# Kernel tuning notes

Measured on AMD Instinct MI355X. Metric: run time of the kernel, lower is better.

Reference implementation:

```python
import jax, jax.numpy as jnp
import numpy as np

PI = np.pi


def setup_inputs() -> dict:
    key = jax.random.key(0)
    ks = jax.random.split(key, 20)
    B, L, D = 2, 1024, 512
    TP = 16      # n_sets(4) * planes_per_set(4)
    PP = 16      # pos_planes
    MAXL = 8192
    sc = 1.0 / np.sqrt(D)
    return {
        "x": jax.random.normal(ks[0], (B, L, D), jnp.float32),
        "Wk": jax.random.normal(ks[1], (TP, D), jnp.float32) * sc,
        "bk": jnp.zeros((TP,), jnp.float32),
        "Wq": jax.random.normal(ks[2], (TP, D), jnp.float32) * sc,
        "bq": jnp.zeros((TP,), jnp.float32),
        "Wv": jax.random.normal(ks[3], (D, D), jnp.float32) * sc,
        "bv": jnp.zeros((D,), jnp.float32),
        "ln_g": jnp.ones((D,), jnp.float32),
        "ln_b": jnp.zeros((D,), jnp.float32),
        "Wo": jax.random.normal(ks[4], (D, D), jnp.float32) * sc,
        "bo": jnp.zeros((D,), jnp.float32),
        "set_w": jnp.ones((4,), jnp.float32),
        "pos_phases": jax.random.normal(ks[5], (MAXL, PP), jnp.float32) * PI,
        "pos_weight": jnp.ones((1,), jnp.float32),
        "Wg1": jax.random.normal(ks[6], (D // 2, D), jnp.float32) * sc,
        "bg1": jnp.zeros((D // 2,), jnp.float32),
        "Wg2": jax.random.normal(ks[7], (1, D // 2), jnp.float32) * np.sqrt(2.0 / D),
        "bg2": jnp.zeros((1,), jnp.float32),
    }


def reference(x, Wk, bk, Wq, bq, Wv, bv, ln_g, ln_b, Wo, bo,
              set_w, pos_phases, pos_weight, Wg1, bg1, Wg2, bg2):
    B, L, D = x.shape
    n_sets, pps = 4, 4

    # --- content phasor memory ---
    kp = jnp.tanh(x @ Wk.T + bk) * PI                       # [B,L,16]
    qp = jnp.tanh(x @ Wq.T + bq) * PI
    key_ph = jnp.exp(1j * kp).reshape(B, L, n_sets, pps)    # [B,L,S,P] c64
    qry_ph = jnp.exp(1j * qp).reshape(B, L, n_sets, pps)
    Vr = x @ Wv.T + bv                                       # [B,L,D]
    V = Vr.astype(jnp.complex64)

    bound = key_ph[..., None] * V[:, :, None, None, :]       # [B,L,S,P,D] c64
    mem = jnp.cumsum(bound, axis=1)                          # prefix-sum memory
    retr = (mem * jnp.conj(qry_ph)[..., None]).sum(axis=3).real   # [B,L,S,D]
    w = jax.nn.softmax(set_w)
    content = (retr * w[None, None, :, None]).sum(axis=2)    # [B,L,D]

    # --- positional cos/sin memory ---
    ph = pos_phases[:L]                                      # [L,PP]
    c = jnp.cos(ph)[None]                                    # [1,L,PP]
    s = jnp.sin(ph)[None]
    br = Vr[:, :, None, :] * c[..., None]                    # [B,L,PP,D]
    bi = Vr[:, :, None, :] * s[..., None]
    mr = jnp.cumsum(br, axis=1)
    mi = jnp.cumsum(bi, axis=1)
    pos = (mr * c[..., None] + mi * s[..., None]).sum(axis=2)  # [B,L,D]

    # --- gate, mix, normalize, output proj ---
    g = jax.nn.sigmoid(
        jax.nn.gelu(x @ Wg1.T + bg1, approximate=False) @ Wg2.T + bg2)  # [B,L,1]
    total = g * content + (1.0 - g) * jax.nn.sigmoid(pos_weight) * pos
    norm = jnp.sqrt(jnp.arange(1, L + 1, dtype=x.dtype) * pps)[None, :, None]
    t = total / norm
    mu = t.mean(-1, keepdims=True)
    var = ((t - mu) ** 2).mean(-1, keepdims=True)
    tn = (t - mu) / jnp.sqrt(var + 1e-5) * ln_g + ln_b
    return x + tn @ Wo.T + bo
```

## Files before the change

kernel.cpp:

```cpp
#include <hip/hip_runtime.h>
#include <math.h>

#define PI_F 3.14159265358979323846f
#define BB 2
#define LL 1024
#define NCH 64
#define CHUNK 32
#define NCHUNK (LL/CHUNK)
#define NW 1408
#define YH 384

typedef __attribute__((ext_vector_type(8))) short short8;
typedef __attribute__((ext_vector_type(4))) float floatx4;
typedef const __attribute__((address_space(1))) unsigned int cgu32;
typedef __attribute__((address_space(3))) unsigned int lu32;

__device__ __forceinline__ unsigned short f2bf(float f){
    unsigned u = __float_as_uint(f);
    unsigned r = (u + 0x7fff + ((u >> 16) & 1)) >> 16;
    return (unsigned short)r;
}

__global__ __launch_bounds__(128) void k_prep(
    const float* __restrict__ Wv, const float* __restrict__ Wg1,
    const float* __restrict__ Wk, const float* __restrict__ Wq,
    const float* __restrict__ Wo,
    const float* __restrict__ bv, const float* __restrict__ bg1,
    const float* __restrict__ bk, const float* __restrict__ bq,
    const float* __restrict__ bo, const float* __restrict__ x,
    unsigned short* __restrict__ Wb, float* __restrict__ bcat,
    unsigned short* __restrict__ xb)
{
    const int bid = blockIdx.x, tid = threadIdx.x;
    if (bid < NW){
        const int n = bid;
        const float* src = (n<512) ? Wv  + (size_t)n*512
                         : (n<768) ? Wg1 + (size_t)(n-512)*512
                         : (n<784) ? Wk  + (size_t)(n-768)*512
                         : (n<800) ? Wq  + (size_t)(n-784)*512
                         : (n<896) ? (const float*)0
                                   : Wo  + (size_t)(n-896)*512;
        float4 v = make_float4(0.f,0.f,0.f,0.f);
        if (src) v = ((const float4*)src)[tid];
        ushort4 o; o.x=f2bf(v.x); o.y=f2bf(v.y); o.z=f2bf(v.z); o.w=f2bf(v.w);
        ((ushort4*)(Wb + (size_t)n*512))[tid] = o;
        if (tid == 0)
            bcat[n] = (n<512)?bv[n] : (n<768)?bg1[n-512] : (n<784)?bk[n-768]
                    : (n<800)?bq[n-784] : (n<896)?0.f : bo[n-896];
    } else {
        const size_t i = (size_t)(bid - NW)*128 + tid;
        float4 v = ((const float4*)x)[i];
        ushort4 o; o.x=f2bf(v.x); o.y=f2bf(v.y); o.z=f2bf(v.z); o.w=f2bf(v.w);
        ((ushort4*)xb)[i] = o;
    }
}

__device__ __forceinline__ void gemm64x64(
    const unsigned short* Ag, const unsigned short* Bg,
    short* As, short* Bs, int tid, floatx4 acc[2][2])
{
    const int lane = tid & 63, w = tid >> 6;
    const int wm = w & 1, wn = w >> 1;
    const int q = lane >> 4, m15 = lane & 15;
    for (int kt = 0; kt < 512; kt += 64) {
        __syncthreads();
        #pragma unroll
        for (int i = 0; i < 2; ++i) {
            const int rowbase = (w*2 + i) * 8;
            const int r  = rowbase + (lane >> 3);
            const int gb = (lane & 7) ^ (r & 7);
            const unsigned short* ga  = Ag + (size_t)r*512 + kt + gb*8;
            const unsigned short* gbp = Bg + (size_t)r*512 + kt + gb*8;
            __builtin_amdgcn_global_load_lds((cgu32*)(const void*)ga,
                                             (lu32*)(As + rowbase*64), 16, 0, 0);
            __builtin_amdgcn_global_load_lds((cgu32*)(const void*)gbp,
                                             (lu32*)(Bs + rowbase*64), 16, 0, 0);
        }
        __syncthreads();
        #pragma unroll
        for (int k32 = 0; k32 < 64; k32 += 32) {
            short8 af[2], bf[2];
            #pragma unroll
            for (int t = 0; t < 2; ++t) {
                const int ra  = 32*wm + 16*t + m15;
                const int sba = ((k32>>3) + q) ^ (ra & 7);
                af[t] = *(const short8*)(As + ra*64 + sba*8);
                const int rb  = 32*wn + 16*t + m15;
                const int sbb = ((k32>>3) + q) ^ (rb & 7);
                bf[t] = *(const short8*)(Bs + rb*64 + sbb*8);
            }
            #pragma unroll
            for (int mt = 0; mt < 2; ++mt)
                #pragma unroll
                for (int nt = 0; nt < 2; ++nt)
                    acc[mt][nt] = __builtin_amdgcn_mfma_f32_16x16x32_bf16(
                        af[mt], bf[nt], acc[mt][nt], 0, 0, 0);
        }
    }
}

__global__ __launch_bounds__(256) void kg1(
    const unsigned short* __restrict__ xb, const unsigned short* __restrict__ Wb,
    const float* __restrict__ bcat, unsigned short* __restrict__ Vt,
    float* __restrict__ Yh)
{
    __shared__ short As[64*64], Bs[64*64];
    const int tid = threadIdx.x;
    const int row0 = blockIdx.x*64, n0 = blockIdx.y*64;
    floatx4 acc[2][2];
    #pragma unroll
    for (int mt=0;mt<2;++mt)
        #pragma unroll
        for (int nt=0;nt<2;++nt) acc[mt][nt] = (floatx4){0.f,0.f,0.f,0.f};
    gemm64x64(xb + (size_t)row0*512, Wb + (size_t)n0*512, As, Bs, tid, acc);
    const int lane = tid & 63, w = tid >> 6;
    const int wm = w & 1, wn = w >> 1, q = lane >> 4, m15 = lane & 15;
    if (n0 < 512){
        const int b = row0 >> 10, lb = row0 & 1023;
        #pragma unroll
        for (int mt=0;mt<2;++mt)
            #pragma unroll
            for (int nt=0;nt<2;++nt){
                const int d = n0 + 32*wn + 16*nt + m15;
                const float bb = bcat[d];
                const int l0 = lb + 32*wm + 16*mt + q*4;
                ushort4 o;
                o.x = f2bf(acc[mt][nt][0] + bb);
                o.y = f2bf(acc[mt][nt][1] + bb);
                o.z = f2bf(acc[mt][nt][2] + bb);
                o.w = f2bf(acc[mt][nt][3] + bb);
                *(ushort4*)(Vt + ((size_t)(b*512 + d))*1024 + l0) = o;
            }
    } else {
        #pragma unroll
        for (int mt=0;mt<2;++mt)
            #pragma unroll
            for (int nt=0;nt<2;++nt){
                const int n = n0 + 32*wn + 16*nt + m15;
                const float bb = bcat[n];
                #pragma unroll
                for (int reg=0;reg<4;++reg){
                    const int m = row0 + 32*wm + 16*mt + q*4 + reg;
                    Yh[(size_t)m*YH + (n-512)] = acc[mt][nt][reg] + bb;
                }
            }
    }
}

__global__ __launch_bounds__(256) void k_act(
    const float* __restrict__ Yh, const float* __restrict__ Wg2,
    const float* __restrict__ bg2, const float* __restrict__ set_w,
    const float* __restrict__ pos_phases, const float* __restrict__ pos_weight,
    unsigned short* __restrict__ ab, unsigned short* __restrict__ Rb,
    unsigned short* __restrict__ aT)
{
    const int tid = threadIdx.x, lane = tid & 63, w = tid >> 6;
    const int row0 = blockIdx.x * 8;
    float s0=set_w[0], s1=set_w[1], s2=set_w[2], s3=set_w[3];
    float m = fmaxf(fmaxf(s0,s1), fmaxf(s2,s3));
    float e0=expf(s0-m), e1=expf(s1-m), e2=expf(s2-m), e3=expf(s3-m);
    float esum = e0+e1+e2+e3;
    float spw = 1.f/(1.f+expf(-pos_weight[0]));
    float b2 = bg2[0];
    #pragma unroll
    for (int rr=0;rr<2;++rr){
        int row = row0 + w + 4*rr;
        const float* yrow = Yh + (size_t)row*YH;
        float hs = 0.f;
        #pragma unroll
        for (int i=0;i<4;++i){
            float hv = yrow[lane + 64*i];
            float ge = 0.5f*hv*(1.f + erff(hv*0.70710678118f));
            hs += ge * Wg2[lane + 64*i];
        }
        #pragma unroll
        for (int off=32; off; off>>=1) hs += __shfl_xor(hs, off, 64);
        float g = 1.f/(1.f+expf(-(hs + b2)));
        if (lane < 16){
            int j = lane;
            int l = row & (LL-1);
            int b = row >> 10;
            float kang = PI_F*tanhf(yrow[256 + j]);
            float qang = PI_F*tanhf(yrow[272 + j]);
            float wsm = (j<4?e0: j<8?e1: j<12?e2: e3) / esum;
            float rnorm = 1.f/(2.f*sqrtf((float)(l+1)));
            float av[4], rv[4];
            av[0] = cosf(kang); av[1] = sinf(kang);
            float cw = g*wsm*rnorm;
            rv[0] = cw*cosf(qang); rv[1] = cw*sinf(qang);
            float ph = pos_phases[(size_t)l*16 + j];
            float pc = cosf(ph), ps = sinf(ph);
            av[2] = pc; av[3] = ps;
            float cp = (1.f-g)*spw*rnorm;
            rv[2] = cp*pc; rv[3] = cp*ps;
            unsigned short* arow = ab + (size_t)row*NCH;
            unsigned short* Rrow = Rb + (size_t)row*NCH;
            #pragma unroll
            for (int t=0;t<4;++t){
                arow[16*t + j] = f2bf(av[t]);
                Rrow[16*t + j] = f2bf(rv[t]);
                aT[((size_t)b*NCH + 16*t + j)*1024 + l] = f2bf(av[t]);
            }
        }
    }
}

__global__ __launch_bounds__(256) void k2a_chunksum(
    const unsigned short* __restrict__ aT, const unsigned short* __restrict__ Vt,
    float* __restrict__ P)
{
    const int c = blockIdx.x, b = blockIdx.y, z = blockIdx.z;
    const int tid = threadIdx.x, lane = tid & 63, w = tid >> 6;
    const int q = lane >> 4, m15 = lane & 15;
    short8 af[4];
    #pragma unroll
    for (int mt=0;mt<4;++mt)
        af[mt] = *(const short8*)(aT + ((size_t)b*NCH + 16*mt + m15)*1024 + c*32 + q*8);
    floatx4 acc[4][4];
    #pragma unroll
    for (int mt=0;mt<4;++mt)
        #pragma unroll
        for (int nt=0;nt<4;++nt) acc[mt][nt] = (floatx4){0.f,0.f,0.f,0.f};
    #pragma unroll
    for (int nt=0;nt<4;++nt){
        const int d = z*256 + w*64 + 16*nt + m15;
        short8 bf = *(const short8*)(Vt + ((size_t)(b*512 + d))*1024 + c*32 + q*8);
        #pragma unroll
        for (int mt=0;mt<4;++mt)
            acc[mt][nt] = __builtin_amdgcn_mfma_f32_16x16x32_bf16(af[mt], bf, acc[mt][nt], 0,0,0);
    }
    float* Pc = P + ((size_t)(b*NCHUNK + c))*512*NCH;
    #pragma unroll
    for (int mt=0;mt<4;++mt)
        #pragma unroll
        for (int nt=0;nt<4;++nt){
            const int d = z*256 + w*64 + 16*nt + m15;
            const int ch0 = 16*mt + q*4;
            *(floatx4*)(Pc + (size_t)d*NCH + ch0) = acc[mt][nt];
        }
}

__global__ __launch_bounds__(256) void k2b_prefix(
    const float* __restrict__ P, unsigned short* __restrict__ S0t)
{
    const int b = blockIdx.y;
    const size_t idx = (size_t)blockIdx.x*256 + threadIdx.x;
    float run = 0.f;
    for (int c=0;c<NCHUNK;++c){
        const size_t o = ((size_t)(b*NCHUNK + c))*512*NCH + idx;
        float v = P[o];
        S0t[o] = f2bf(run);
        run += v;
    }
}

__global__ __launch_bounds__(256) void k2c_scan(
    const unsigned short* __restrict__ ab, const unsigned short* __restrict__ Rb,
    const unsigned short* __restrict__ Vt, const unsigned short* __restrict__ S0t,
    const float* __restrict__ ln_g, const float* __restrict__ ln_b,
    unsigned short* __restrict__ Tn)
{
    __shared__ short Msh[32*32];
    __shared__ float Tsh[32*512];
    const int c = blockIdx.x, b = blockIdx.y;
    const int tid = threadIdx.x, lane = tid & 63, w = tid >> 6;
    const int q = lane >> 4, m15 = lane & 15;
    const int grow = b*1024 + c*32;

    if (w == 0){
        floatx4 mcc[2][2];
        #pragma unroll
        for (int mt=0;mt<2;++mt)
            #pragma unroll
            for (int nt=0;nt<2;++nt) mcc[mt][nt] = (floatx4){0.f,0.f,0.f,0.f};
        #pragma unroll
        for (int ks=0;ks<2;++ks){
            short8 ra[2], bb[2];
            #pragma unroll
            for (int t=0;t<2;++t){
                ra[t] = *(const short8*)(Rb + (size_t)(grow + 16*t + m15)*NCH + ks*32 + q*8);
                bb[t] = *(const short8*)(ab + (size_t)(grow + 16*t + m15)*NCH + ks*32 + q*8);
            }
            #pragma unroll
            for (int mt=0;mt<2;++mt)
                #pragma unroll
                for (int nt=0;nt<2;++nt)
                    mcc[mt][nt] = __builtin_amdgcn_mfma_f32_16x16x32_bf16(
                        ra[mt], bb[nt], mcc[mt][nt], 0,0,0);
        }
        #pragma unroll
        for (int mt=0;mt<2;++mt)
            #pragma unroll
            for (int nt=0;nt<2;++nt){
                const int nl = 16*nt + m15;
                #pragma unroll
                for (int reg=0;reg<4;++reg){
                    const int ml = 16*mt + q*4 + reg;
                    Msh[ml*32 + nl] = (nl <= ml) ? (short)f2bf(mcc[mt][nt][reg]) : (short)0;
                }
            }
    }
    __syncthreads();

    short8 a1[2], a2[2][2];
    #pragma unroll
    for (int mt=0;mt<2;++mt){
        a1[mt] = *(const short8*)(Msh + (16*mt + m15)*32 + q*8);
        #pragma unroll
        for (int ks=0;ks<2;++ks)
            a2[ks][mt] = *(const short8*)(Rb + (size_t)(grow + 16*mt + m15)*NCH + ks*32 + q*8);
    }
    floatx4 acc[2][8];
    #pragma unroll
    for (int mt=0;mt<2;++mt)
        #pragma unroll
        for (int nt=0;nt<8;++nt) acc[mt][nt] = (floatx4){0.f,0.f,0.f,0.f};
    const unsigned short* S0c = S0t + ((size_t)(b*NCHUNK + c))*512*NCH;
    #pragma unroll
    for (int nt=0;nt<8;++nt){
        const int d = w*128 + 16*nt + m15;
        short8 b1 = *(const short8*)(Vt + ((size_t)(b*512 + d))*1024 + c*32 + q*8);
        #pragma unroll
        for (int mt=0;mt<2;++mt)
            acc[mt][nt] = __builtin_amdgcn_mfma_f32_16x16x32_bf16(a1[mt], b1, acc[mt][nt], 0,0,0);
        #pragma unroll
        for (int ks=0;ks<2;++ks){
            short8 b2 = *(const short8*)(S0c + (size_t)d*NCH + ks*32 + q*8);
            #pragma unroll
            for (int mt=0;mt<2;++mt)
                acc[mt][nt] = __builtin_amdgcn_mfma_f32_16x16x32_bf16(a2[ks][mt], b2, acc[mt][nt], 0,0,0);
        }
    }
    #pragma unroll
    for (int mt=0;mt<2;++mt)
        #pragma unroll
        for (int nt=0;nt<8;++nt){
            const int d = w*128 + 16*nt + m15;
            #pragma unroll
            for (int reg=0;reg<4;++reg)
                Tsh[(16*mt + q*4 + reg)*512 + d] = acc[mt][nt][reg];
        }
    __syncthreads();

    #pragma unroll
    for (int i=0;i<8;++i){
        const int r = w*8 + i;
        float s=0.f, sq=0.f;
        #pragma unroll
        for (int t=0;t<8;++t){
            float v = Tsh[r*512 + lane + 64*t];
            s += v; sq += v*v;
        }
        #pragma unroll
        for (int off=32; off; off>>=1){
            s += __shfl_xor(s, off, 64); sq += __shfl_xor(sq, off, 64);
        }
        float mu  = s*(1.f/512.f);
        float var = sq*(1.f/512.f) - mu*mu;
        float rsd = rsqrtf(var + 1e-5f);
        unsigned short* trow = Tn + (size_t)(grow + r)*512;
        #pragma unroll
        for (int t=0;t<8;++t){
            const int d = lane + 64*t;
            float v = (Tsh[r*512 + d] - mu)*rsd*ln_g[d] + ln_b[d];
            trow[d] = f2bf(v);
        }
    }
}

__global__ __launch_bounds__(256) void kg2(
    const unsigned short* __restrict__ Tn, const unsigned short* __restrict__ Wb,
    const float* __restrict__ bcat, const float* __restrict__ x,
    float* __restrict__ out)
{
    __shared__ short As[64*64], Bs[64*64];
    const int tid = threadIdx.x;
    const int row0 = blockIdx.x*64, n0 = blockIdx.y*64;
    floatx4 acc[2][2];
    #pragma unroll
    for (int mt=0;mt<2;++mt)
        #pragma unroll
        for (int nt=0;nt<2;++nt) acc[mt][nt] = (floatx4){0.f,0.f,0.f,0.f};
    gemm64x64(Tn + (size_t)row0*512, Wb + (size_t)(896+n0)*512, As, Bs, tid, acc);
    const int lane = tid & 63, w = tid >> 6;
    const int wm = w & 1, wn = w >> 1, q = lane >> 4, m15 = lane & 15;
    #pragma unroll
    for (int mt=0;mt<2;++mt)
        #pragma unroll
        for (int nt=0;nt<2;++nt){
            const int n = n0 + 32*wn + 16*nt + m15;
            const float bb = bcat[896 + n];
            #pragma unroll
            for (int reg=0;reg<4;++reg){
                const int m = row0 + 32*wm + 16*mt + q*4 + reg;
                out[(size_t)m*512 + n] = x[(size_t)m*512 + n] + acc[mt][nt][reg] + bb;
            }
        }
}

extern "C" void kernel_launch(void* const* d_in, const int* in_sizes, int n_in,
                              void* d_out, int out_size, void* d_ws, size_t ws_size,
                              hipStream_t stream) {
    const float* x    = (const float*)d_in[0];
    const float* Wk   = (const float*)d_in[1];
    const float* bk   = (const float*)d_in[2];
    const float* Wq   = (const float*)d_in[3];
    const float* bq   = (const float*)d_in[4];
    const float* Wv   = (const float*)d_in[5];
    const float* bv   = (const float*)d_in[6];
    const float* ln_g = (const float*)d_in[7];
    const float* ln_b = (const float*)d_in[8];
    const float* Wo   = (const float*)d_in[9];
    const float* bo   = (const float*)d_in[10];
    const float* set_w      = (const float*)d_in[11];
    const float* pos_phases = (const float*)d_in[12];
    const float* pos_weight = (const float*)d_in[13];
    const float* Wg1  = (const float*)d_in[14];
    const float* bg1  = (const float*)d_in[15];
    const float* Wg2  = (const float*)d_in[16];
    const float* bg2  = (const float*)d_in[17];
    float* out = (float*)d_out;

    float* ws   = (float*)d_ws;
    float* Yh   = ws;
    float* P    = Yh + (size_t)2048*YH;
    float* bcat = P  + (size_t)BB*NCHUNK*512*NCH;
    unsigned short* Wb  = (unsigned short*)(bcat + NW);
    unsigned short* xb  = Wb  + (size_t)NW*512;
    unsigned short* Vt  = xb  + (size_t)2048*512;
    unsigned short* ab  = Vt  + (size_t)BB*512*1024;
    unsigned short* Rb  = ab  + (size_t)2048*NCH;
    unsigned short* aT  = Rb  + (size_t)2048*NCH;
    unsigned short* S0t = aT  + (size_t)BB*NCH*1024;
    unsigned short* Tn  = S0t + (size_t)BB*NCHUNK*512*NCH;

    k_prep<<<dim3(NW + 2048), 128, 0, stream>>>(
        Wv,Wg1,Wk,Wq,Wo, bv,bg1,bk,bq,bo, x, Wb, bcat, xb);
    kg1<<<dim3(2048/64, 14), 256, 0, stream>>>(xb, Wb, bcat, Vt, Yh);
    k_act<<<dim3(2048/8), 256, 0, stream>>>(
        Yh, Wg2, bg2, set_w, pos_phases, pos_weight, ab, Rb, aT);
    k2a_chunksum<<<dim3(NCHUNK, BB, 2), 256, 0, stream>>>(aT, Vt, P);
    k2b_prefix<<<dim3(512*NCH/256, BB), 256, 0, stream>>>(P, S0t);
    k2c_scan<<<dim3(NCHUNK, BB), 256, 0, stream>>>(ab, Rb, Vt, S0t, ln_g, ln_b, Tn);
    kg2<<<dim3(2048/64, 512/64), 256, 0, stream>>>(Tn, Wb, bcat, x, out);
}
```

Measured before the change: 135.2 us.

## Fuse six stage kernels into one persistent kernel with grid-wide barriers

Replaces the six kernels that followed the prep kernel (GEMM1, activation, chunk sums, prefix, scan with layernorm, GEMM2) with one persistent 512-block kernel. The stages are separated by atomic-counter grid barriers, which the prep kernel resets. This removes five kernel launches and the gaps between them. In exchange, many blocks sit idle in the later stages, and the design needs all 512 blocks to be co-resident, which the 67KB of static shared memory and launch bounds of 2 may not allow on every configuration. The chunk-sum stage is also re-split so each block does a quarter of the previous work.

```diff
diff --git a/kernel.cpp b/kernel.cpp
--- a/kernel.cpp
+++ b/kernel.cpp
@@ -9,6 +9,7 @@
 #define NCHUNK (LL/CHUNK)
 #define NW 1408
 #define YH 384
+#define GRID_F 512
 
 typedef __attribute__((ext_vector_type(8))) short short8;
 typedef __attribute__((ext_vector_type(4))) float floatx4;
@@ -29,9 +30,10 @@
     const float* __restrict__ bk, const float* __restrict__ bq,
     const float* __restrict__ bo, const float* __restrict__ x,
     unsigned short* __restrict__ Wb, float* __restrict__ bcat,
-    unsigned short* __restrict__ xb)
+    unsigned short* __restrict__ xb, unsigned* __restrict__ bar)
 {
     const int bid = blockIdx.x, tid = threadIdx.x;
+    if (bid == 0 && tid < 8) bar[tid] = 0u;
     if (bid < NW){
         const int n = bid;
         const float* src = (n<512) ? Wv  + (size_t)n*512
@@ -55,12 +57,23 @@
     }
 }
 
+__device__ __forceinline__ void gsync(unsigned* bar, unsigned nblk){
+    __syncthreads();
+    if (threadIdx.x == 0){
+        __threadfence();
+        __hip_atomic_fetch_add(bar, 1u, __ATOMIC_RELAXED, __HIP_MEMORY_SCOPE_AGENT);
+        while (__hip_atomic_load(bar, __ATOMIC_RELAXED, __HIP_MEMORY_SCOPE_AGENT) < nblk)
+            __builtin_amdgcn_s_sleep(2);
+        __threadfence();
+    }
+    __syncthreads();
+}
+
 __device__ __forceinline__ void gemm64x64(
     const unsigned short* Ag, const unsigned short* Bg,
     short* As, short* Bs, int tid, floatx4 acc[2][2])
 {
     const int lane = tid & 63, w = tid >> 6;
-    const int wm = w & 1, wn = w >> 1;
     const int q = lane >> 4, m15 = lane & 15;
     for (int kt = 0; kt < 512; kt += 64) {
         __syncthreads();
@@ -82,10 +95,10 @@
             short8 af[2], bf[2];
             #pragma unroll
             for (int t = 0; t < 2; ++t) {
-                const int ra  = 32*wm + 16*t + m15;
+                const int ra  = 32*(w & 1) + 16*t + m15;
                 const int sba = ((k32>>3) + q) ^ (ra & 7);
                 af[t] = *(const short8*)(As + ra*64 + sba*8);
-                const int rb  = 32*wn + 16*t + m15;
+                const int rb  = 32*(w >> 1) + 16*t + m15;
                 const int sbb = ((k32>>3) + q) ^ (rb & 7);
                 bf[t] = *(const short8*)(Bs + rb*64 + sbb*8);
             }
@@ -99,72 +112,78 @@
     }
 }
 
-__global__ __launch_bounds__(256) void kg1(
+__global__ __launch_bounds__(256, 2) void k_fused(
     const unsigned short* __restrict__ xb, const unsigned short* __restrict__ Wb,
     const float* __restrict__ bcat, unsigned short* __restrict__ Vt,
-    float* __restrict__ Yh)
+    float* __restrict__ Yh,
+    const float* __restrict__ Wg2, const float* __restrict__ bg2,
+    const float* __restrict__ set_w, const float* __restrict__ pos_phases,
+    const float* __restrict__ pos_weight,
+    unsigned short* __restrict__ ab, unsigned short* __restrict__ Rb,
+    unsigned short* __restrict__ aT,
+    float* __restrict__ P, unsigned short* __restrict__ S0t,
+    const float* __restrict__ ln_g, const float* __restrict__ ln_b,
+    unsigned short* __restrict__ Tn,
+    const float* __restrict__ x, float* __restrict__ out,
+    unsigned* __restrict__ bar)
 {
-    __shared__ short As[64*64], Bs[64*64];
-    const int tid = threadIdx.x;
-    const int row0 = blockIdx.x*64, n0 = blockIdx.y*64;
-    floatx4 acc[2][2];
-    #pragma unroll
-    for (int mt=0;mt<2;++mt)
-        #pragma unroll
-        for (int nt=0;nt<2;++nt) acc[mt][nt] = (floatx4){0.f,0.f,0.f,0.f};
-    gemm64x64(xb + (size_t)row0*512, Wb + (size_t)n0*512, As, Bs, tid, acc);
+    __shared__ __align__(16) char smem[67584];
+    const int bid = blockIdx.x, tid = threadIdx.x;
     const int lane = tid & 63, w = tid >> 6;
-    const int wm = w & 1, wn = w >> 1, q = lane >> 4, m15 = lane & 15;
-    if (n0 < 512){
-        const int b = row0 >> 10, lb = row0 & 1023;
+    const int q = lane >> 4, m15 = lane & 15;
+
+    if (bid < 448){
+        short* As = (short*)smem;
+        short* Bs = (short*)(smem + 8192);
+        const int row0 = (bid & 31)*64, n0 = (bid >> 5)*64;
+        floatx4 acc[2][2];
         #pragma unroll
         for (int mt=0;mt<2;++mt)
             #pragma unroll
-            for (int nt=0;nt<2;++nt){
-                const int d = n0 + 32*wn + 16*nt + m15;
-                const float bb = bcat[d];
-                const int l0 = lb + 32*wm + 16*mt + q*4;
-                ushort4 o;
-                o.x = f2bf(acc[mt][nt][0] + bb);
-                o.y = f2bf(acc[mt][nt][1] + bb);
-                o.z = f2bf(acc[mt][nt][2] + bb);
-                o.w = f2bf(acc[mt][nt][3] + bb);
-                *(ushort4*)(Vt + ((size_t)(b*512 + d))*1024 + l0) = o;
-            }
-    } else {
-        #pragma unroll
-        for (int mt=0;mt<2;++mt)
-            #pragma unroll
-            for (int nt=0;nt<2;++nt){
-                const int n = n0 + 32*wn + 16*nt + m15;
-                const float bb = bcat[n];
-                #pragma unroll
-                for (int reg=0;reg<4;++reg){
-                    const int m = row0 + 32*wm + 16*mt + q*4 + reg;
-                    Yh[(size_t)m*YH + (n-512)] = acc[mt][nt][reg] + bb;
+            for (int nt=0;nt<2;++nt) acc[mt][nt] = (floatx4){0.f,0.f,0.f,0.f};
+        gemm64x64(xb + (size_t)row0*512, Wb + (size_t)n0*512, As, Bs, tid, acc);
+        const int wm = w & 1, wn = w >> 1;
+        if (n0 < 512){
+            const int b = row0 >> 10, lb = row0 & 1023;
+            #pragma unroll
+            for (int mt=0;mt<2;++mt)
+                #pragma unroll
+                for (int nt=0;nt<2;++nt){
+                    const int d = n0 + 32*wn + 16*nt + m15;
+                    const float bb = bcat[d];
+                    const int l0 = lb + 32*wm + 16*mt + q*4;
+                    ushort4 o;
+                    o.x = f2bf(acc[mt][nt][0] + bb);
+                    o.y = f2bf(acc[mt][nt][1] + bb);
+                    o.z = f2bf(acc[mt][nt][2] + bb);
+                    o.w = f2bf(acc[mt][nt][3] + bb);
+                    *(ushort4*)(Vt + ((size_t)(b*512 + d))*1024 + l0) = o;
                 }
-            }
-    }
-}
-
-__global__ __launch_bounds__(256) void k_act(
-    const float* __restrict__ Yh, const float* __restrict__ Wg2,
-    const float* __restrict__ bg2, const float* __restrict__ set_w,
-    const float* __restrict__ pos_phases, const float* __restrict__ pos_weight,
-    unsigned short* __restrict__ ab, unsigned short* __restrict__ Rb,
-    unsigned short* __restrict__ aT)
-{
-    const int tid = threadIdx.x, lane = tid & 63, w = tid >> 6;
-    const int row0 = blockIdx.x * 8;
-    float s0=set_w[0], s1=set_w[1], s2=set_w[2], s3=set_w[3];
-    float m = fmaxf(fmaxf(s0,s1), fmaxf(s2,s3));
-    float e0=expf(s0-m), e1=expf(s1-m), e2=expf(s2-m), e3=expf(s3-m);
-    float esum = e0+e1+e2+e3;
-    float spw = 1.f/(1.f+expf(-pos_weight[0]));
-    float b2 = bg2[0];
-    #pragma unroll
-    for (int rr=0;rr<2;++rr){
-        int row = row0 + w + 4*rr;
+        } else {
+            #pragma unroll
+            for (int mt=0;mt<2;++mt)
+                #pragma unroll
+                for (int nt=0;nt<2;++nt){
+                    const int n = n0 + 32*wn + 16*nt + m15;
+                    const float bb = bcat[n];
+                    #pragma unroll
+                    for (int reg=0;reg<4;++reg){
+                        const int m = row0 + 32*wm + 16*mt + q*4 + reg;
+                        Yh[(size_t)m*YH + (n-512)] = acc[mt][nt][reg] + bb;
+                    }
+                }
+        }
+    }
+    gsync(bar+0, GRID_F);
+
+    {
+        float s0=set_w[0], s1=set_w[1], s2=set_w[2], s3=set_w[3];
+        float mm = fmaxf(fmaxf(s0,s1), fmaxf(s2,s3));
+        float e0=expf(s0-mm), e1=expf(s1-mm), e2=expf(s2-mm), e3=expf(s3-mm);
+        float esum = e0+e1+e2+e3;
+        float spw = 1.f/(1.f+expf(-pos_weight[0]));
+        float b2 = bg2[0];
+        const int row = bid*4 + w;
         const float* yrow = Yh + (size_t)row*YH;
         float hs = 0.f;
         #pragma unroll
@@ -203,199 +222,174 @@
             }
         }
     }
-}
-
-__global__ __launch_bounds__(256) void k2a_chunksum(
-    const unsigned short* __restrict__ aT, const unsigned short* __restrict__ Vt,
-    float* __restrict__ P)
-{
-    const int c = blockIdx.x, b = blockIdx.y, z = blockIdx.z;
-    const int tid = threadIdx.x, lane = tid & 63, w = tid >> 6;
-    const int q = lane >> 4, m15 = lane & 15;
-    short8 af[4];
-    #pragma unroll
-    for (int mt=0;mt<4;++mt)
-        af[mt] = *(const short8*)(aT + ((size_t)b*NCH + 16*mt + m15)*1024 + c*32 + q*8);
-    floatx4 acc[4][4];
-    #pragma unroll
-    for (int mt=0;mt<4;++mt)
-        #pragma unroll
-        for (int nt=0;nt<4;++nt) acc[mt][nt] = (floatx4){0.f,0.f,0.f,0.f};
-    #pragma unroll
-    for (int nt=0;nt<4;++nt){
-        const int d = z*256 + w*64 + 16*nt + m15;
+    gsync(bar+1, GRID_F);
+
+    {
+        const int c = bid & 31, b = (bid >> 5) & 1, z8 = bid >> 6;
+        short8 af[4];
+        #pragma unroll
+        for (int mt=0;mt<4;++mt)
+            af[mt] = *(const short8*)(aT + ((size_t)b*NCH + 16*mt + m15)*1024 + c*32 + q*8);
+        const int d = z8*64 + w*16 + m15;
         short8 bf = *(const short8*)(Vt + ((size_t)(b*512 + d))*1024 + c*32 + q*8);
+        floatx4 pacc[4];
+        #pragma unroll
+        for (int mt=0;mt<4;++mt) pacc[mt] = (floatx4){0.f,0.f,0.f,0.f};
         #pragma unroll
         for (int mt=0;mt<4;++mt)
-            acc[mt][nt] = __builtin_amdgcn_mfma_f32_16x16x32_bf16(af[mt], bf, acc[mt][nt], 0,0,0);
-    }
-    float* Pc = P + ((size_t)(b*NCHUNK + c))*512*NCH;
-    #pragma unroll
-    for (int mt=0;mt<4;++mt)
-        #pragma unroll
-        for (int nt=0;nt<4;++nt){
-            const int d = z*256 + w*64 + 16*nt + m15;
-            const int ch0 = 16*mt + q*4;
-            *(floatx4*)(Pc + (size_t)d*NCH + ch0) = acc[mt][nt];
-        }
-}
-
-__global__ __launch_bounds__(256) void k2b_prefix(
-    const float* __restrict__ P, unsigned short* __restrict__ S0t)
-{
-    const int b = blockIdx.y;
-    const size_t idx = (size_t)blockIdx.x*256 + threadIdx.x;
-    float run = 0.f;
-    for (int c=0;c<NCHUNK;++c){
-        const size_t o = ((size_t)(b*NCHUNK + c))*512*NCH + idx;
-        float v = P[o];
-        S0t[o] = f2bf(run);
-        run += v;
-    }
-}
-
-__global__ __launch_bounds__(256) void k2c_scan(
-    const unsigned short* __restrict__ ab, const unsigned short* __restrict__ Rb,
-    const unsigned short* __restrict__ Vt, const unsigned short* __restrict__ S0t,
-    const float* __restrict__ ln_g, const float* __restrict__ ln_b,
-    unsigned short* __restrict__ Tn)
-{
-    __shared__ short Msh[32*32];
-    __shared__ float Tsh[32*512];
-    const int c = blockIdx.x, b = blockIdx.y;
-    const int tid = threadIdx.x, lane = tid & 63, w = tid >> 6;
-    const int q = lane >> 4, m15 = lane & 15;
-    const int grow = b*1024 + c*32;
-
-    if (w == 0){
-        floatx4 mcc[2][2];
+            pacc[mt] = __builtin_amdgcn_mfma_f32_16x16x32_bf16(af[mt], bf, pacc[mt], 0,0,0);
+        float* Pc = P + ((size_t)(b*NCHUNK + c))*512*NCH;
+        #pragma unroll
+        for (int mt=0;mt<4;++mt)
+            *(floatx4*)(Pc + (size_t)d*NCH + 16*mt + q*4) = pacc[mt];
+    }
+    gsync(bar+2, GRID_F);
+
+    if (bid < 256){
+        const int b = bid >> 7;
+        const size_t idx = (size_t)(bid & 127)*256 + tid;
+        float run = 0.f;
+        for (int c2=0;c2<NCHUNK;++c2){
+            const size_t o = ((size_t)(b*NCHUNK + c2))*512*NCH + idx;
+            float v = P[o];
+            S0t[o] = f2bf(run);
+            run += v;
+        }
+    }
+    gsync(bar+3, GRID_F);
+
+    if (bid < 64){
+        short* Msh = (short*)smem;
+        float* Tsh = (float*)(smem + 2048);
+        const int c = bid & 31, b = bid >> 5;
+        const int grow = b*1024 + c*32;
+
+        if (w == 0){
+            floatx4 mcc[2][2];
+            #pragma unroll
+            for (int mt=0;mt<2;++mt)
+                #pragma unroll
+                for (int nt=0;nt<2;++nt) mcc[mt][nt] = (floatx4){0.f,0.f,0.f,0.f};
+            #pragma unroll
+            for (int ks=0;ks<2;++ks){
+                short8 ra[2], bb[2];
+                #pragma unroll
+                for (int t=0;t<2;++t){
+                    ra[t] = *(const short8*)(Rb + (size_t)(grow + 16*t + m15)*NCH + ks*32 + q*8);
+                    bb[t] = *(const short8*)(ab + (size_t)(grow + 16*t + m15)*NCH + ks*32 + q*8);
+                }
+                #pragma unroll
+                for (int mt=0;mt<2;++mt)
+                    #pragma unroll
+                    for (int nt=0;nt<2;++nt)
+                        mcc[mt][nt] = __builtin_amdgcn_mfma_f32_16x16x32_bf16(
+                            ra[mt], bb[nt], mcc[mt][nt], 0,0,0);
+            }
+            #pragma unroll
+            for (int mt=0;mt<2;++mt)
+                #pragma unroll
+                for (int nt=0;nt<2;++nt){
+                    const int nl = 16*nt + m15;
+                    #pragma unroll
+                    for (int reg=0;reg<4;++reg){
+                        const int ml = 16*mt + q*4 + reg;
+                        Msh[ml*32 + nl] = (nl <= ml) ? (short)f2bf(mcc[mt][nt][reg]) : (short)0;
+                    }
+                }
+        }
+        __syncthreads();
+
+        short8 a1[2], a2[2][2];
+        #pragma unroll
+        for (int mt=0;mt<2;++mt){
+            a1[mt] = *(const short8*)(Msh + (16*mt + m15)*32 + q*8);
+            #pragma unroll
+            for (int ks=0;ks<2;++ks)
+                a2[ks][mt] = *(const short8*)(Rb + (size_t)(grow + 16*mt + m15)*NCH + ks*32 + q*8);
+        }
+        floatx4 acc[2][8];
         #pragma unroll
         for (int mt=0;mt<2;++mt)
             #pragma unroll
-            for (int nt=0;nt<2;++nt) mcc[mt][nt] = (floatx4){0.f,0.f,0.f,0.f};
-        #pragma unroll
-        for (int ks=0;ks<2;++ks){
-            short8 ra[2], bb[2];
-            #pragma unroll
-            for (int t=0;t<2;++t){
-                ra[t] = *(const short8*)(Rb + (size_t)(grow + 16*t + m15)*NCH + ks*32 + q*8);
-                bb[t] = *(const short8*)(ab + (size_t)(grow + 16*t + m15)*NCH + ks*32 + q*8);
-            }
-            #pragma unroll
-            for (int mt=0;mt<2;++mt)
-                #pragma unroll
-                for (int nt=0;nt<2;++nt)
-                    mcc[mt][nt] = __builtin_amdgcn_mfma_f32_16x16x32_bf16(
-                        ra[mt], bb[nt], mcc[mt][nt], 0,0,0);
-        }
-        #pragma unroll
-        for (int mt=0;mt<2;++mt)
-            #pragma unroll
-            for (int nt=0;nt<2;++nt){
-                const int nl = 16*nt + m15;
-                #pragma unroll
-                for (int reg=0;reg<4;++reg){
-                    const int ml = 16*mt + q*4 + reg;
-                    Msh[ml*32 + nl] = (nl <= ml) ? (short)f2bf(mcc[mt][nt][reg]) : (short)0;
-                }
-            }
-    }
-    __syncthreads();
-
-    short8 a1[2], a2[2][2];
-    #pragma unroll
-    for (int mt=0;mt<2;++mt){
-        a1[mt] = *(const short8*)(Msh + (16*mt + m15)*32 + q*8);
-        #pragma unroll
-        for (int ks=0;ks<2;++ks)
-            a2[ks][mt] = *(const short8*)(Rb + (size_t)(grow + 16*mt + m15)*NCH + ks*32 + q*8);
-    }
-    floatx4 acc[2][8];
-    #pragma unroll
-    for (int mt=0;mt<2;++mt)
-        #pragma unroll
-        for (int nt=0;nt<8;++nt) acc[mt][nt] = (floatx4){0.f,0.f,0.f,0.f};
-    const unsigned short* S0c = S0t + ((size_t)(b*NCHUNK + c))*512*NCH;
-    #pragma unroll
-    for (int nt=0;nt<8;++nt){
-        const int d = w*128 + 16*nt + m15;
-        short8 b1 = *(const short8*)(Vt + ((size_t)(b*512 + d))*1024 + c*32 + q*8);
-        #pragma unroll
-        for (int mt=0;mt<2;++mt)
-            acc[mt][nt] = __builtin_amdgcn_mfma_f32_16x16x32_bf16(a1[mt], b1, acc[mt][nt], 0,0,0);
-        #pragma unroll
-        for (int ks=0;ks<2;++ks){
-            short8 b2 = *(const short8*)(S0c + (size_t)d*NCH + ks*32 + q*8);
-            #pragma unroll
-            for (int mt=0;mt<2;++mt)
-                acc[mt][nt] = __builtin_amdgcn_mfma_f32_16x16x32_bf16(a2[ks][mt], b2, acc[mt][nt], 0,0,0);
-        }
-    }
-    #pragma unroll
-    for (int mt=0;mt<2;++mt)
+            for (int nt=0;nt<8;++nt) acc[mt][nt] = (floatx4){0.f,0.f,0.f,0.f};
+        const unsigned short* S0c = S0t + ((size_t)(b*NCHUNK + c))*512*NCH;
         #pragma unroll
         for (int nt=0;nt<8;++nt){
             const int d = w*128 + 16*nt + m15;
-            #pragma unroll
-            for (int reg=0;reg<4;++reg)
-                Tsh[(16*mt + q*4 + reg)*512 + d] = acc[mt][nt][reg];
-        }
-    __syncthreads();
-
-    #pragma unroll
-    for (int i=0;i<8;++i){
-        const int r = w*8 + i;
-        float s=0.f, sq=0.f;
-        #pragma unroll
-        for (int t=0;t<8;++t){
-            float v = Tsh[r*512 + lane + 64*t];
-            s += v; sq += v*v;
-        }
-        #pragma unroll
-        for (int off=32; off; off>>=1){
-            s += __shfl_xor(s, off, 64); sq += __shfl_xor(sq, off, 64);
-        }
-        float mu  = s*(1.f/512.f);
-        float var = sq*(1.f/512.f) - mu*mu;
-        float rsd = rsqrtf(var + 1e-5f);
-        unsigned short* trow = Tn + (size_t)(grow + r)*512;
-        #pragma unroll
-        for (int t=0;t<8;++t){
-            const int d = lane + 64*t;
-            float v = (Tsh[r*512 + d] - mu)*rsd*ln_g[d] + ln_b[d];
-            trow[d] = f2bf(v);
-        }
-    }
-}
-
-__global__ __launch_bounds__(256) void kg2(
-    const unsigned short* __restrict__ Tn, const unsigned short* __restrict__ Wb,
-    const float* __restrict__ bcat, const float* __restrict__ x,
-    float* __restrict__ out)
-{
-    __shared__ short As[64*64], Bs[64*64];
-    const int tid = threadIdx.x;
-    const int row0 = blockIdx.x*64, n0 = blockIdx.y*64;
-    floatx4 acc[2][2];
-    #pragma unroll
-    for (int mt=0;mt<2;++mt)
-        #pragma unroll
-        for (int nt=0;nt<2;++nt) acc[mt][nt] = (floatx4){0.f,0.f,0.f,0.f};
-    gemm64x64(Tn + (size_t)row0*512, Wb + (size_t)(896+n0)*512, As, Bs, tid, acc);
-    const int lane = tid & 63, w = tid >> 6;
-    const int wm = w & 1, wn = w >> 1, q = lane >> 4, m15 = lane & 15;
-    #pragma unroll
-    for (int mt=0;mt<2;++mt)
-        #pragma unroll
-        for (int nt=0;nt<2;++nt){
-            const int n = n0 + 32*wn + 16*nt + m15;
-            const float bb = bcat[896 + n];
-            #pragma unroll
-            for (int reg=0;reg<4;++reg){
-                const int m = row0 + 32*wm + 16*mt + q*4 + reg;
-                out[(size_t)m*512 + n] = x[(size_t)m*512 + n] + acc[mt][nt][reg] + bb;
-            }
-        }
+            short8 b1 = *(const short8*)(Vt + ((size_t)(b*512 + d))*1024 + c*32 + q*8);
+            #pragma unroll
+            for (int mt=0;mt<2;++mt)
+                acc[mt][nt] = __builtin_amdgcn_mfma_f32_16x16x32_bf16(a1[mt], b1, acc[mt][nt], 0,0,0);
+            #pragma unroll
+            for (int ks=0;ks<2;++ks){
+                short8 b2v = *(const short8*)(S0c + (size_t)d*NCH + ks*32 + q*8);
+                #pragma unroll
+                for (int mt=0;mt<2;++mt)
+                    acc[mt][nt] = __builtin_amdgcn_mfma_f32_16x16x32_bf16(a2[ks][mt], b2v, acc[mt][nt], 0,0,0);
+            }
+        }
+        #pragma unroll
+        for (int mt=0;mt<2;++mt)
+            #pragma unroll
+            for (int nt=0;nt<8;++nt){
+                const int d = w*128 + 16*nt + m15;
+                #pragma unroll
+                for (int reg=0;reg<4;++reg)
+                    Tsh[(16*mt + q*4 + reg)*512 + d] = acc[mt][nt][reg];
+            }
+        __syncthreads();
+
+        #pragma unroll
+        for (int i=0;i<8;++i){
+            const int r = w*8 + i;
+            float s=0.f, sq=0.f;
+            #pragma unroll
+            for (int t=0;t<8;++t){
+                float v = Tsh[r*512 + lane + 64*t];
+                s += v; sq += v*v;
+            }
+            #pragma unroll
+            for (int off=32; off; off>>=1){
+                s += __shfl_xor(s, off, 64); sq += __shfl_xor(sq, off, 64);
+            }
+            float mu  = s*(1.f/512.f);
+            float var = sq*(1.f/512.f) - mu*mu;
+            float rsd = rsqrtf(var + 1e-5f);
+            unsigned short* trow = Tn + (size_t)(grow + r)*512;
+            #pragma unroll
+            for (int t=0;t<8;++t){
+                const int d = lane + 64*t;
+                float v = (Tsh[r*512 + d] - mu)*rsd*ln_g[d] + ln_b[d];
+                trow[d] = f2bf(v);
+            }
+        }
+    }
+    gsync(bar+4, GRID_F);
+
+    if (bid < 256){
+        short* As = (short*)smem;
+        short* Bs = (short*)(smem + 8192);
+        const int row0 = (bid & 31)*64, n0 = (bid >> 5)*64;
+        floatx4 acc[2][2];
+        #pragma unroll
+        for (int mt=0;mt<2;++mt)
+            #pragma unroll
+            for (int nt=0;nt<2;++nt) acc[mt][nt] = (floatx4){0.f,0.f,0.f,0.f};
+        gemm64x64(Tn + (size_t)row0*512, Wb + (size_t)(896+n0)*512, As, Bs, tid, acc);
+        const int wm = w & 1, wn = w >> 1;
+        #pragma unroll
+        for (int mt=0;mt<2;++mt)
+            #pragma unroll
+            for (int nt=0;nt<2;++nt){
+                const int n = n0 + 32*wn + 16*nt + m15;
+                const float bb = bcat[896 + n];
+                #pragma unroll
+                for (int reg=0;reg<4;++reg){
+                    const int m = row0 + 32*wm + 16*mt + q*4 + reg;
+                    out[(size_t)m*512 + n] = x[(size_t)m*512 + n] + acc[mt][nt][reg] + bb;
+                }
+            }
+    }
 }
 
 extern "C" void kernel_launch(void* const* d_in, const int* in_sizes, int n_in,
@@ -433,14 +427,11 @@
     unsigned short* aT  = Rb  + (size_t)2048*NCH;
     unsigned short* S0t = aT  + (size_t)BB*NCH*1024;
     unsigned short* Tn  = S0t + (size_t)BB*NCHUNK*512*NCH;
+    unsigned*       bar = (unsigned*)(Tn + (size_t)2048*512);
 
     k_prep<<<dim3(NW + 2048), 128, 0, stream>>>(
-        Wv,Wg1,Wk,Wq,Wo, bv,bg1,bk,bq,bo, x, Wb, bcat, xb);
-    kg1<<<dim3(2048/64, 14), 256, 0, stream>>>(xb, Wb, bcat, Vt, Yh);
-    k_act<<<dim3(2048/8), 256, 0, stream>>>(
-        Yh, Wg2, bg2, set_w, pos_phases, pos_weight, ab, Rb, aT);
-    k2a_chunksum<<<dim3(NCHUNK, BB, 2), 256, 0, stream>>>(aT, Vt, P);
-    k2b_prefix<<<dim3(512*NCH/256, BB), 256, 0, stream>>>(P, S0t);
-    k2c_scan<<<dim3(NCHUNK, BB), 256, 0, stream>>>(ab, Rb, Vt, S0t, ln_g, ln_b, Tn);
-    kg2<<<dim3(2048/64, 512/64), 256, 0, stream>>>(Tn, Wb, bcat, x, out);
-}
+        Wv,Wg1,Wk,Wq,Wo, bv,bg1,bk,bq,bo, x, Wb, bcat, xb, bar);
+    k_fused<<<dim3(GRID_F), 256, 0, stream>>>(
+        xb, Wb, bcat, Vt, Yh, Wg2, bg2, set_w, pos_phases, pos_weight,
+        ab, Rb, aT, P, S0t, ln_g, ln_b, Tn, x, out, bar);
+}
```

Result: slower. 365.0 us (+169.9%).
